# Performance work log

Hardware: AMD Instinct MI355X
Metric: run time of the kernel (lower is better)

The kernel has to match this reference:

```python
import jax, jax.numpy as jnp
import numpy as np

N_USER, N_ITEM, N_BUNDLE = 200000, 100000, 50000
EMBED_DIM = 128
B, L = 8192, 100  # batch of bundles, max items per bundle


def setup_inputs() -> dict:
    key = jax.random.key(0)
    ks = jax.random.split(key, 12)
    d, d2 = EMBED_DIM, 2 * EMBED_DIM
    x_u = jax.random.randint(ks[0], (B,), 0, N_USER)
    x_b = jax.random.randint(ks[1], (B,), 0, N_BUNDLE)
    items = jax.random.randint(ks[2], (B, L), 0, N_ITEM)
    # ragged bundle sizes in [10, L]; padded+masked form of the CSR gather
    lengths = jax.random.randint(ks[3], (B,), 10, L + 1)
    mask = jnp.arange(L)[None, :] < lengths[:, None]  # [B, L] bool
    return {
        "x_u": x_u,
        "x_b": x_b,
        "items": items,
        "mask": mask,
        "emb_u": jax.random.normal(ks[4], (N_USER, d), jnp.float32) * 0.1,
        "emb_i": jax.random.normal(ks[5], (N_ITEM, d), jnp.float32) * 0.1,
        "emb_b": jax.random.normal(ks[6], (N_BUNDLE, d), jnp.float32) * 0.1,
        "A": jax.random.normal(ks[7], (N_ITEM, d), jnp.float32) * 0.1,
        "fc1_w": jax.random.normal(ks[8], (d2, d2), jnp.float32) / np.sqrt(d2),
        "fc1_b": jnp.zeros((d2,), jnp.float32),
        "fc2_w": jax.random.normal(ks[9], (d2, d2), jnp.float32) / np.sqrt(d2),
        "fc2_b": jnp.zeros((d2,), jnp.float32),
        "out_w": jax.random.normal(ks[10], (1, d2), jnp.float32) / np.sqrt(d2),
        "out_b": jnp.zeros((1,), jnp.float32),
    }


def reference(x_u, x_b, items, mask, emb_u, emb_i, emb_b, A,
              fc1_w, fc1_b, fc2_w, fc2_b, out_w, out_b):
    # DAM.forward_bundle with the attention() per-bundle loop vectorized
    h_u = emb_u[x_u]                       # [B, d]
    h_b = emb_b[x_b]                       # [B, d]
    item_e = emb_i[items]                  # [B, L, d] ragged gather (padded)
    a_e = A[items]                         # [B, L, d]
    # w = softmax_l( sum_d e_u * A[item] ) per bundle, over valid items only
    scores = jnp.einsum('bd,bld->bl', h_u, a_e)
    scores = jnp.where(mask, scores, -jnp.inf)
    w = jax.nn.softmax(scores, axis=1)     # [B, L]
    h_x = jnp.einsum('bl,bld->bd', w, item_e)
    h = jnp.concatenate([h_u, h_b + h_x], axis=1)   # [B, 2d]
    h = jax.nn.leaky_relu(h @ fc1_w.T + fc1_b)
    h = jax.nn.leaky_relu(h @ fc2_w.T + fc2_b)
    return h @ out_w.T + out_b             # [B, 1]
```

## Files before the change

### kernel.cpp

```cpp
#include <hip/hip_runtime.h>
#include <hip/hip_bf16.h>

#define D   128
#define D2  256

typedef short bf16x8 __attribute__((ext_vector_type(8)));
typedef float f32x4  __attribute__((ext_vector_type(4)));

__device__ __forceinline__ float bf2f(unsigned short u) {
    return __uint_as_float(((unsigned int)u) << 16);
}
__device__ __forceinline__ float bflo(unsigned int p) { return __uint_as_float(p << 16); }
__device__ __forceinline__ float bfhi(unsigned int p) { return __uint_as_float(p & 0xffff0000u); }
__device__ __forceinline__ unsigned short f2bf(float f) {
    __hip_bfloat16 h = __float2bfloat16(f);
    return *(unsigned short*)&h;
}

template<bool BF>
__device__ __forceinline__ float ld1(const void* p, size_t i) {
    if constexpr (BF) return bf2f(((const unsigned short*)p)[i]);
    else              return ((const float*)p)[i];
}

template<bool BF>
__device__ __forceinline__ void load8f(const void* p, size_t elem_off, float* r) {
    if constexpr (BF) {
        uint4 v = *(const uint4*)((const unsigned short*)p + elem_off);
        r[0]=bflo(v.x); r[1]=bfhi(v.x); r[2]=bflo(v.y); r[3]=bfhi(v.y);
        r[4]=bflo(v.z); r[5]=bfhi(v.z); r[6]=bflo(v.w); r[7]=bfhi(v.w);
    } else {
        const float4* q = (const float4*)((const float*)p + elem_off);
        float4 a = q[0], b = q[1];
        r[0]=a.x; r[1]=a.y; r[2]=a.z; r[3]=a.w;
        r[4]=b.x; r[5]=b.y; r[6]=b.z; r[7]=b.w;
    }
}

__global__ void detect_kernel(const unsigned int* __restrict__ probe,
                              const unsigned char* __restrict__ mask,
                              int* __restrict__ flags)
{
    const int t = threadIdx.x;
    int cnt = 0;
    for (int i = t; i < 256; i += 64) {
        unsigned int e = (probe[i] >> 7) & 0xffu;
        cnt += (e >= 90 && e < 130) ? 1 : 0;
    }
    #pragma unroll
    for (int o = 32; o; o >>= 1) cnt += __shfl_xor(cnt, o);
    if (t == 0) {
        flags[0] = (cnt >= 128) ? 1 : 0;
        flags[1] = (mask[1] == 0) ? 0 : ((mask[0] == 1) ? 1 : 2);
    }
}

template<bool BF>
__device__ __forceinline__ void attn_body(
    const int* __restrict__ x_u, const int* __restrict__ x_b,
    const int* __restrict__ items, const void* __restrict__ mask, int mmode,
    const void* __restrict__ emb_u, const void* __restrict__ emb_i,
    const void* __restrict__ emb_b, const void* __restrict__ Aw,
    unsigned short* __restrict__ h_out, int L)
{
    const int b  = blockIdx.x;
    const int t  = threadIdx.x;
    const int wv = t >> 6, ln = t & 63;

    __shared__ float hu_s[D];
    __shared__ float sc_s[128];
    __shared__ float w_s[128];
    __shared__ int   it_s[128];
    __shared__ int   cnt_s[4];
    __shared__ float redm_s[4];
    __shared__ float reds_s[4];
    __shared__ float part_s[16][D];

    const int xu = x_u[b], xb = x_b[b];
    float hu = 0.f;
    if (t < D) { hu = ld1<BF>(emb_u, (size_t)xu * D + t); hu_s[t] = hu; }

    bool valid = false;
    if (t < L && t < 128) {
        const size_t mi = (size_t)b * L + t;
        it_s[t] = items[mi];
        if (mmode == 0)      valid = ((const int*)mask)[mi] != 0;
        else if (mmode == 1) valid = ((const unsigned char*)mask)[mi] != 0;
        else                 valid = ((const unsigned short*)mask)[mi] != 0;
    }
    unsigned long long bm = __ballot(valid);
    if (ln == 0) cnt_s[wv] = __popcll(bm);
    __syncthreads();
    const int len = cnt_s[0] + cnt_s[1] + cnt_s[2] + cnt_s[3];

    const int item = t >> 1, half = t & 1;
    if (item < len) {
        float acc = 0.f, r[8];
        const size_t base = (size_t)it_s[item] * D + half * 64;
        const float4* hu4 = (const float4*)hu_s + half * 16;
        #pragma unroll
        for (int c = 0; c < 8; ++c) {
            load8f<BF>(Aw, base + 8 * c, r);
            float4 ha = hu4[2 * c], hb2 = hu4[2 * c + 1];
            acc += ha.x * r[0] + ha.y * r[1] + ha.z * r[2] + ha.w * r[3]
                 + hb2.x * r[4] + hb2.y * r[5] + hb2.z * r[6] + hb2.w * r[7];
        }
        acc += __shfl_xor(acc, 1);
        if (half == 0) sc_s[item] = acc;
    }
    if (t >= len && t < 128) it_s[t] = it_s[0];
    __syncthreads();

    const float s = (t < len) ? sc_s[t] : -INFINITY;
    float mx = s;
    #pragma unroll
    for (int o = 32; o; o >>= 1) mx = fmaxf(mx, __shfl_xor(mx, o));
    if (ln == 0) redm_s[wv] = mx;
    __syncthreads();
    mx = fmaxf(fmaxf(redm_s[0], redm_s[1]), fmaxf(redm_s[2], redm_s[3]));
    const float e = (t < len) ? __expf(s - mx) : 0.f;
    float sm = e;
    #pragma unroll
    for (int o = 32; o; o >>= 1) sm += __shfl_xor(sm, o);
    if (ln == 0) reds_s[wv] = sm;
    __syncthreads();
    sm = reds_s[0] + reds_s[1] + reds_s[2] + reds_s[3];
    const float inv = (sm > 0.f) ? 1.f / sm : 0.f;
    if (t < 128) w_s[t] = e * inv;
    __syncthreads();

    const int g = t >> 4, m16 = t & 15;
    const int nit = (len + 31) & ~31;
    float acc[8];
    #pragma unroll
    for (int k = 0; k < 8; ++k) acc[k] = 0.f;
    for (int i = 0; i < nit; i += 32) {
        const int l0 = i + g, l1 = i + 16 + g;
        const float w0 = w_s[l0], w1 = w_s[l1];
        float r0[8], r1[8];
        load8f<BF>(emb_i, (size_t)it_s[l0] * D + 8 * m16, r0);
        load8f<BF>(emb_i, (size_t)it_s[l1] * D + 8 * m16, r1);
        #pragma unroll
        for (int k = 0; k < 8; ++k) acc[k] += w0 * r0[k] + w1 * r1[k];
    }
    #pragma unroll
    for (int k = 0; k < 8; ++k) part_s[g][8 * m16 + k] = acc[k];
    __syncthreads();

    if (t < D) {
        float hx = 0.f;
        #pragma unroll
        for (int gg = 0; gg < 16; ++gg) hx += part_s[gg][t];
        const float hbv = ld1<BF>(emb_b, (size_t)xb * D + t);
        h_out[(size_t)b * D2 + t]     = f2bf(hu);
        h_out[(size_t)b * D2 + D + t] = f2bf(hbv + hx);
    }
}

__global__ __launch_bounds__(256) void attn_kernel(
    const int* x_u, const int* x_b, const int* items, const void* mask,
    const void* emb_u, const void* emb_i, const void* emb_b, const void* A,
    unsigned short* h_out, int L, const int* __restrict__ flags)
{
    if (flags[0]) attn_body<true >(x_u, x_b, items, mask, flags[1], emb_u, emb_i, emb_b, A, h_out, L);
    else          attn_body<false>(x_u, x_b, items, mask, flags[1], emb_u, emb_i, emb_b, A, h_out, L);
}

template<bool BF>
__device__ __forceinline__ bf16x8 load_w8(const void* W, size_t off) {
    if constexpr (BF) {
        return *(const bf16x8*)((const unsigned short*)W + off);
    } else {
        const float* p = (const float*)W + off;
        float4 a = *(const float4*)p;
        float4 b = *(const float4*)(p + 4);
        bf16x8 r;
        r[0] = (short)f2bf(a.x); r[1] = (short)f2bf(a.y);
        r[2] = (short)f2bf(a.z); r[3] = (short)f2bf(a.w);
        r[4] = (short)f2bf(b.x); r[5] = (short)f2bf(b.y);
        r[6] = (short)f2bf(b.z); r[7] = (short)f2bf(b.w);
        return r;
    }
}

template<bool BF>
__device__ __forceinline__ void fc_body(
    const unsigned short* __restrict__ X, const void* __restrict__ W,
    const void* __restrict__ bias, unsigned short* __restrict__ Y)
{
    const int tid  = threadIdx.x;
    const int wave = tid >> 6;
    const int lane = tid & 63;
    const int l16  = lane & 15;
    const int quad = lane >> 4;
    const int mt   = blockIdx.x * 16;

    bf16x8 afrag[8];
    const size_t abase = (size_t)(mt + l16) * D2 + quad * 8;
    #pragma unroll
    for (int kc = 0; kc < 8; ++kc)
        afrag[kc] = *(const bf16x8*)(X + abase + kc * 32);

    #pragma unroll
    for (int jj = 0; jj < 4; ++jj) {
        const int jt = wave * 4 + jj;
        const size_t bbase = (size_t)(jt * 16 + l16) * D2 + quad * 8;
        f32x4 acc = {0.f, 0.f, 0.f, 0.f};
        #pragma unroll
        for (int kc = 0; kc < 8; ++kc) {
            bf16x8 bfrag = load_w8<BF>(W, bbase + kc * 32);
            acc = __builtin_amdgcn_mfma_f32_16x16x32_bf16(afrag[kc], bfrag, acc, 0, 0, 0);
        }
        const int j  = jt * 16 + l16;
        const float bj = ld1<BF>(bias, j);
        #pragma unroll
        for (int r = 0; r < 4; ++r) {
            float v = acc[r] + bj;
            v = v > 0.f ? v : 0.01f * v;
            Y[(size_t)(mt + quad * 4 + r) * D2 + j] = f2bf(v);
        }
    }
}

__global__ __launch_bounds__(256) void fc_mfma_kernel(
    const unsigned short* X, const void* W, const void* bias,
    unsigned short* Y, const int* __restrict__ flags)
{
    if (flags[0]) fc_body<true >(X, W, bias, Y);
    else          fc_body<false>(X, W, bias, Y);
}

template<bool BF>
__device__ __forceinline__ void out_body(
    const unsigned short* __restrict__ X, const void* __restrict__ out_w,
    const void* __restrict__ out_b, void* __restrict__ out, int B)
{
    const int gid  = blockIdx.x * blockDim.x + threadIdx.x;
    const int row  = gid >> 6;
    const int lane = threadIdx.x & 63;
    if (row >= B) return;

    const uint2 xv = ((const uint2*)(X + (size_t)row * D2))[lane];
    const float x0 = bflo(xv.x), x1 = bfhi(xv.x), x2 = bflo(xv.y), x3 = bfhi(xv.y);
    float w0, w1, w2, w3;
    if constexpr (BF) {
        uint2 wv = ((const uint2*)out_w)[lane];
        w0 = bflo(wv.x); w1 = bfhi(wv.x); w2 = bflo(wv.y); w3 = bfhi(wv.y);
    } else {
        float4 wv = ((const float4*)out_w)[lane];
        w0 = wv.x; w1 = wv.y; w2 = wv.z; w3 = wv.w;
    }
    float acc = x0 * w0 + x1 * w1 + x2 * w2 + x3 * w3;
    #pragma unroll
    for (int off = 32; off; off >>= 1) acc += __shfl_down(acc, off);
    if (lane == 0) {
        const float v = acc + ld1<BF>(out_b, 0);
        if constexpr (BF) ((unsigned short*)out)[row] = f2bf(v);
        else              ((float*)out)[row] = v;
    }
}

__global__ __launch_bounds__(256) void out_kernel(
    const unsigned short* X, const void* out_w, const void* out_b,
    void* out, int B, const int* __restrict__ flags)
{
    if (flags[0]) out_body<true >(X, out_w, out_b, out, B);
    else          out_body<false>(X, out_w, out_b, out, B);
}

extern "C" void kernel_launch(void* const* d_in, const int* in_sizes, int n_in,
                              void* d_out, int out_size, void* d_ws, size_t ws_size,
                              hipStream_t stream) {
    const int*  x_u   = (const int*)d_in[0];
    const int*  x_b   = (const int*)d_in[1];
    const int*  items = (const int*)d_in[2];
    const void* mask  = d_in[3];
    const void* emb_u = d_in[4];
    const void* emb_i = d_in[5];
    const void* emb_b = d_in[6];
    const void* A     = d_in[7];
    const void* fc1_w = d_in[8];
    const void* fc1_b = d_in[9];
    const void* fc2_w = d_in[10];
    const void* fc2_b = d_in[11];
    const void* out_w = d_in[12];
    const void* out_b = d_in[13];

    const int B = in_sizes[0];
    const int L = in_sizes[2] / B;

    unsigned short* h  = (unsigned short*)d_ws;
    unsigned short* h1 = h + (size_t)B * D2;
    int* flags = (int*)(h1 + (size_t)B * D2);

    detect_kernel<<<1, 64, 0, stream>>>((const unsigned int*)emb_u,
                                        (const unsigned char*)mask, flags);
    attn_kernel<<<B, 256, 0, stream>>>(x_u, x_b, items, mask,
                                       emb_u, emb_i, emb_b, A, h, L, flags);
    fc_mfma_kernel<<<B / 16, 256, 0, stream>>>(h,  fc1_w, fc1_b, h1, flags);
    fc_mfma_kernel<<<B / 16, 256, 0, stream>>>(h1, fc2_w, fc2_b, h,  flags);
    out_kernel<<<B / 4, 256, 0, stream>>>(h, out_w, out_b, d_out, B, flags);
}
```

Baseline: 329.4 us.

## Fuse MLP layers into one kernel, inline dtype probe, prefetch item rows

The separate detect kernel is removed; each attention and MLP block now runs the dtype and mask probe itself into shared memory. fc1, fc2 and the output projection are fused into one kernel that keeps the hidden activations in padded shared memory, which drops two launches and the global round trips for the intermediates. In the bf16 path the attention kernel issues the emb_i gathers for all 128 slots before the softmax so they overlap the reductions, and the softmax now skips the max-subtraction pass and its barrier. Skipping the max subtraction risks overflow if scores grow large, and every block now repeats the small probe read.

```diff
diff --git a/kernel.cpp b/kernel.cpp
--- a/kernel.cpp
+++ b/kernel.cpp
@@ -3,6 +3,7 @@
 
 #define D   128
 #define D2  256
+#define H1P 272
 
 typedef short bf16x8 __attribute__((ext_vector_type(8)));
 typedef float f32x4  __attribute__((ext_vector_type(4)));
@@ -37,22 +38,16 @@
     }
 }
 
-__global__ void detect_kernel(const unsigned int* __restrict__ probe,
-                              const unsigned char* __restrict__ mask,
-                              int* __restrict__ flags)
-{
-    const int t = threadIdx.x;
+__device__ __forceinline__ int probe_bf16(const unsigned int* probe, int lane) {
     int cnt = 0;
-    for (int i = t; i < 256; i += 64) {
-        unsigned int e = (probe[i] >> 7) & 0xffu;
+    #pragma unroll
+    for (int i = 0; i < 4; ++i) {
+        unsigned int e = (probe[lane + 64 * i] >> 7) & 0xffu;
         cnt += (e >= 90 && e < 130) ? 1 : 0;
     }
     #pragma unroll
     for (int o = 32; o; o >>= 1) cnt += __shfl_xor(cnt, o);
-    if (t == 0) {
-        flags[0] = (cnt >= 128) ? 1 : 0;
-        flags[1] = (mask[1] == 0) ? 0 : ((mask[0] == 1) ? 1 : 2);
-    }
+    return cnt;
 }
 
 template<bool BF>
@@ -61,20 +56,13 @@
     const int* __restrict__ items, const void* __restrict__ mask, int mmode,
     const void* __restrict__ emb_u, const void* __restrict__ emb_i,
     const void* __restrict__ emb_b, const void* __restrict__ Aw,
-    unsigned short* __restrict__ h_out, int L)
+    unsigned short* __restrict__ h_out, int L,
+    float* hu_s, float* sc_s, float* w_s, int* it_s,
+    int* cnt_s, float* reds_s, float (*part_s)[132])
 {
     const int b  = blockIdx.x;
     const int t  = threadIdx.x;
     const int wv = t >> 6, ln = t & 63;
-
-    __shared__ float hu_s[D];
-    __shared__ float sc_s[128];
-    __shared__ float w_s[128];
-    __shared__ int   it_s[128];
-    __shared__ int   cnt_s[4];
-    __shared__ float redm_s[4];
-    __shared__ float reds_s[4];
-    __shared__ float part_s[16][D];
 
     const int xu = x_u[b], xb = x_b[b];
     float hu = 0.f;
@@ -111,14 +99,20 @@
     if (t >= len && t < 128) it_s[t] = it_s[0];
     __syncthreads();
 
-    const float s = (t < len) ? sc_s[t] : -INFINITY;
-    float mx = s;
-    #pragma unroll
-    for (int o = 32; o; o >>= 1) mx = fmaxf(mx, __shfl_xor(mx, o));
-    if (ln == 0) redm_s[wv] = mx;
-    __syncthreads();
-    mx = fmaxf(fmaxf(redm_s[0], redm_s[1]), fmaxf(redm_s[2], redm_s[3]));
-    const float e = (t < len) ? __expf(s - mx) : 0.f;
+    const int g = t >> 4, m16 = t & 15;
+
+    uint4 pre0[4], pre1[4];
+    if constexpr (BF) {
+        const unsigned short* EI = (const unsigned short*)emb_i;
+        #pragma unroll
+        for (int i = 0; i < 4; ++i) {
+            pre0[i] = *(const uint4*)(EI + (size_t)it_s[32 * i + g]      * D + 8 * m16);
+            pre1[i] = *(const uint4*)(EI + (size_t)it_s[32 * i + 16 + g] * D + 8 * m16);
+        }
+    }
+
+    const float e = (t < len) ? __expf(sc_s[t]) : 0.f;
+    if (t < 128) w_s[t] = e;
     float sm = e;
     #pragma unroll
     for (int o = 32; o; o >>= 1) sm += __shfl_xor(sm, o);
@@ -126,25 +120,39 @@
     __syncthreads();
     sm = reds_s[0] + reds_s[1] + reds_s[2] + reds_s[3];
     const float inv = (sm > 0.f) ? 1.f / sm : 0.f;
-    if (t < 128) w_s[t] = e * inv;
-    __syncthreads();
-
-    const int g = t >> 4, m16 = t & 15;
-    const int nit = (len + 31) & ~31;
-    float acc[8];
-    #pragma unroll
-    for (int k = 0; k < 8; ++k) acc[k] = 0.f;
-    for (int i = 0; i < nit; i += 32) {
-        const int l0 = i + g, l1 = i + 16 + g;
-        const float w0 = w_s[l0], w1 = w_s[l1];
-        float r0[8], r1[8];
-        load8f<BF>(emb_i, (size_t)it_s[l0] * D + 8 * m16, r0);
-        load8f<BF>(emb_i, (size_t)it_s[l1] * D + 8 * m16, r1);
-        #pragma unroll
-        for (int k = 0; k < 8; ++k) acc[k] += w0 * r0[k] + w1 * r1[k];
-    }
-    #pragma unroll
-    for (int k = 0; k < 8; ++k) part_s[g][8 * m16 + k] = acc[k];
+
+    float acc8[8];
+    #pragma unroll
+    for (int k = 0; k < 8; ++k) acc8[k] = 0.f;
+    if constexpr (BF) {
+        #pragma unroll
+        for (int i = 0; i < 4; ++i) {
+            const float w0 = w_s[32 * i + g], w1 = w_s[32 * i + 16 + g];
+            const uint4 p0 = pre0[i], p1 = pre1[i];
+            acc8[0] += w0 * bflo(p0.x) + w1 * bflo(p1.x);
+            acc8[1] += w0 * bfhi(p0.x) + w1 * bfhi(p1.x);
+            acc8[2] += w0 * bflo(p0.y) + w1 * bflo(p1.y);
+            acc8[3] += w0 * bfhi(p0.y) + w1 * bfhi(p1.y);
+            acc8[4] += w0 * bflo(p0.z) + w1 * bflo(p1.z);
+            acc8[5] += w0 * bfhi(p0.z) + w1 * bfhi(p1.z);
+            acc8[6] += w0 * bflo(p0.w) + w1 * bflo(p1.w);
+            acc8[7] += w0 * bfhi(p0.w) + w1 * bfhi(p1.w);
+        }
+    } else {
+        const int nit = (len + 31) & ~31;
+        for (int i = 0; i < nit; i += 32) {
+            const float w0 = w_s[i + g], w1 = w_s[i + 16 + g];
+            float r0[8], r1[8];
+            load8f<false>(emb_i, (size_t)it_s[i + g] * D + 8 * m16, r0);
+            load8f<false>(emb_i, (size_t)it_s[i + 16 + g] * D + 8 * m16, r1);
+            #pragma unroll
+            for (int k = 0; k < 8; ++k) acc8[k] += w0 * r0[k] + w1 * r1[k];
+        }
+    }
+    f32x4 v0 = {acc8[0] * inv, acc8[1] * inv, acc8[2] * inv, acc8[3] * inv};
+    f32x4 v1 = {acc8[4] * inv, acc8[5] * inv, acc8[6] * inv, acc8[7] * inv};
+    *(f32x4*)&part_s[g][8 * m16]     = v0;
+    *(f32x4*)&part_s[g][8 * m16 + 4] = v1;
     __syncthreads();
 
     if (t < D) {
@@ -160,10 +168,32 @@
 __global__ __launch_bounds__(256) void attn_kernel(
     const int* x_u, const int* x_b, const int* items, const void* mask,
     const void* emb_u, const void* emb_i, const void* emb_b, const void* A,
-    unsigned short* h_out, int L, const int* __restrict__ flags)
+    unsigned short* h_out, int L)
 {
-    if (flags[0]) attn_body<true >(x_u, x_b, items, mask, flags[1], emb_u, emb_i, emb_b, A, h_out, L);
-    else          attn_body<false>(x_u, x_b, items, mask, flags[1], emb_u, emb_i, emb_b, A, h_out, L);
+    __shared__ float hu_s[D];
+    __shared__ float sc_s[128];
+    __shared__ float w_s[128];
+    __shared__ int   it_s[128];
+    __shared__ int   cnt_s[4];
+    __shared__ float reds_s[4];
+    __shared__ float part_s[16][132];
+    __shared__ int   flag_s[2];
+
+    const int t = threadIdx.x;
+    if (t < 64) {
+        int cnt = probe_bf16((const unsigned int*)emb_u, t);
+        if (t == 0) {
+            const unsigned char* mb = (const unsigned char*)mask;
+            flag_s[0] = (cnt >= 128) ? 1 : 0;
+            flag_s[1] = (mb[1] == 0) ? 0 : ((mb[0] == 1) ? 1 : 2);
+        }
+    }
+    __syncthreads();
+
+    if (flag_s[0]) attn_body<true >(x_u, x_b, items, mask, flag_s[1], emb_u, emb_i, emb_b, A,
+                                    h_out, L, hu_s, sc_s, w_s, it_s, cnt_s, reds_s, part_s);
+    else           attn_body<false>(x_u, x_b, items, mask, flag_s[1], emb_u, emb_i, emb_b, A,
+                                    h_out, L, hu_s, sc_s, w_s, it_s, cnt_s, reds_s, part_s);
 }
 
 template<bool BF>
@@ -184,9 +214,13 @@
 }
 
 template<bool BF>
-__device__ __forceinline__ void fc_body(
-    const unsigned short* __restrict__ X, const void* __restrict__ W,
-    const void* __restrict__ bias, unsigned short* __restrict__ Y)
+__device__ __forceinline__ void mlp_body(
+    const unsigned short* __restrict__ X,
+    const void* __restrict__ fc1_w, const void* __restrict__ fc1_b,
+    const void* __restrict__ fc2_w, const void* __restrict__ fc2_b,
+    const void* __restrict__ out_w, const void* __restrict__ out_b,
+    void* __restrict__ out,
+    unsigned short* h1_s, float (*po_s)[16])
 {
     const int tid  = threadIdx.x;
     const int wave = tid >> 6;
@@ -208,64 +242,83 @@
         f32x4 acc = {0.f, 0.f, 0.f, 0.f};
         #pragma unroll
         for (int kc = 0; kc < 8; ++kc) {
-            bf16x8 bfrag = load_w8<BF>(W, bbase + kc * 32);
+            bf16x8 bfrag = load_w8<BF>(fc1_w, bbase + kc * 32);
             acc = __builtin_amdgcn_mfma_f32_16x16x32_bf16(afrag[kc], bfrag, acc, 0, 0, 0);
         }
         const int j  = jt * 16 + l16;
-        const float bj = ld1<BF>(bias, j);
+        const float bj = ld1<BF>(fc1_b, j);
         #pragma unroll
         for (int r = 0; r < 4; ++r) {
             float v = acc[r] + bj;
             v = v > 0.f ? v : 0.01f * v;
-            Y[(size_t)(mt + quad * 4 + r) * D2 + j] = f2bf(v);
-        }
-    }
-}
-
-__global__ __launch_bounds__(256) void fc_mfma_kernel(
-    const unsigned short* X, const void* W, const void* bias,
-    unsigned short* Y, const int* __restrict__ flags)
+            h1_s[(quad * 4 + r) * H1P + j] = f2bf(v);
+        }
+    }
+    __syncthreads();
+
+    bf16x8 afrag2[8];
+    #pragma unroll
+    for (int kc = 0; kc < 8; ++kc)
+        afrag2[kc] = *(const bf16x8*)&h1_s[l16 * H1P + quad * 8 + kc * 32];
+
+    float po[4] = {0.f, 0.f, 0.f, 0.f};
+    #pragma unroll
+    for (int jj = 0; jj < 4; ++jj) {
+        const int jt = wave * 4 + jj;
+        const size_t bbase = (size_t)(jt * 16 + l16) * D2 + quad * 8;
+        f32x4 acc = {0.f, 0.f, 0.f, 0.f};
+        #pragma unroll
+        for (int kc = 0; kc < 8; ++kc) {
+            bf16x8 bfrag = load_w8<BF>(fc2_w, bbase + kc * 32);
+            acc = __builtin_amdgcn_mfma_f32_16x16x32_bf16(afrag2[kc], bfrag, acc, 0, 0, 0);
+        }
+        const int j  = jt * 16 + l16;
+        const float bj = ld1<BF>(fc2_b, j);
+        const float wj = ld1<BF>(out_w, j);
+        #pragma unroll
+        for (int r = 0; r < 4; ++r) {
+            float v = acc[r] + bj;
+            v = v > 0.f ? v : 0.01f * v;
+            po[r] += v * wj;
+        }
+    }
+    #pragma unroll
+    for (int r = 0; r < 4; ++r) {
+        #pragma unroll
+        for (int o = 1; o < 16; o <<= 1) po[r] += __shfl_xor(po[r], o);
+    }
+    if (l16 == 0) {
+        #pragma unroll
+        for (int r = 0; r < 4; ++r) po_s[wave][quad * 4 + r] = po[r];
+    }
+    __syncthreads();
+
+    if (tid < 16) {
+        const float v = po_s[0][tid] + po_s[1][tid] + po_s[2][tid] + po_s[3][tid]
+                      + ld1<BF>(out_b, 0);
+        if constexpr (BF) ((unsigned short*)out)[mt + tid] = f2bf(v);
+        else              ((float*)out)[mt + tid] = v;
+    }
+}
+
+__global__ __launch_bounds__(256) void mlp_kernel(
+    const unsigned short* X,
+    const void* fc1_w, const void* fc1_b, const void* fc2_w, const void* fc2_b,
+    const void* out_w, const void* out_b, void* out, const void* probe)
 {
-    if (flags[0]) fc_body<true >(X, W, bias, Y);
-    else          fc_body<false>(X, W, bias, Y);
-}
-
-template<bool BF>
-__device__ __forceinline__ void out_body(
-    const unsigned short* __restrict__ X, const void* __restrict__ out_w,
-    const void* __restrict__ out_b, void* __restrict__ out, int B)
-{
-    const int gid  = blockIdx.x * blockDim.x + threadIdx.x;
-    const int row  = gid >> 6;
-    const int lane = threadIdx.x & 63;
-    if (row >= B) return;
-
-    const uint2 xv = ((const uint2*)(X + (size_t)row * D2))[lane];
-    const float x0 = bflo(xv.x), x1 = bfhi(xv.x), x2 = bflo(xv.y), x3 = bfhi(xv.y);
-    float w0, w1, w2, w3;
-    if constexpr (BF) {
-        uint2 wv = ((const uint2*)out_w)[lane];
-        w0 = bflo(wv.x); w1 = bfhi(wv.x); w2 = bflo(wv.y); w3 = bfhi(wv.y);
-    } else {
-        float4 wv = ((const float4*)out_w)[lane];
-        w0 = wv.x; w1 = wv.y; w2 = wv.z; w3 = wv.w;
-    }
-    float acc = x0 * w0 + x1 * w1 + x2 * w2 + x3 * w3;
-    #pragma unroll
-    for (int off = 32; off; off >>= 1) acc += __shfl_down(acc, off);
-    if (lane == 0) {
-        const float v = acc + ld1<BF>(out_b, 0);
-        if constexpr (BF) ((unsigned short*)out)[row] = f2bf(v);
-        else              ((float*)out)[row] = v;
-    }
-}
-
-__global__ __launch_bounds__(256) void out_kernel(
-    const unsigned short* X, const void* out_w, const void* out_b,
-    void* out, int B, const int* __restrict__ flags)
-{
-    if (flags[0]) out_body<true >(X, out_w, out_b, out, B);
-    else          out_body<false>(X, out_w, out_b, out, B);
+    __shared__ unsigned short h1_s[16 * H1P];
+    __shared__ float po_s[4][16];
+    __shared__ int flag_s;
+
+    const int t = threadIdx.x;
+    if (t < 64) {
+        int cnt = probe_bf16((const unsigned int*)probe, t);
+        if (t == 0) flag_s = (cnt >= 128) ? 1 : 0;
+    }
+    __syncthreads();
+
+    if (flag_s) mlp_body<true >(X, fc1_w, fc1_b, fc2_w, fc2_b, out_w, out_b, out, h1_s, po_s);
+    else        mlp_body<false>(X, fc1_w, fc1_b, fc2_w, fc2_b, out_w, out_b, out, h1_s, po_s);
 }
 
 extern "C" void kernel_launch(void* const* d_in, const int* in_sizes, int n_in,
@@ -289,15 +342,10 @@
     const int B = in_sizes[0];
     const int L = in_sizes[2] / B;
 
-    unsigned short* h  = (unsigned short*)d_ws;
-    unsigned short* h1 = h + (size_t)B * D2;
-    int* flags = (int*)(h1 + (size_t)B * D2);
-
-    detect_kernel<<<1, 64, 0, stream>>>((const unsigned int*)emb_u,
-                                        (const unsigned char*)mask, flags);
+    unsigned short* h = (unsigned short*)d_ws;
+
     attn_kernel<<<B, 256, 0, stream>>>(x_u, x_b, items, mask,
-                                       emb_u, emb_i, emb_b, A, h, L, flags);
-    fc_mfma_kernel<<<B / 16, 256, 0, stream>>>(h,  fc1_w, fc1_b, h1, flags);
-    fc_mfma_kernel<<<B / 16, 256, 0, stream>>>(h1, fc2_w, fc2_b, h,  flags);
-    out_kernel<<<B / 4, 256, 0, stream>>>(h, out_w, out_b, d_out, B, flags);
-}
+                                       emb_u, emb_i, emb_b, A, h, L);
+    mlp_kernel<<<B / 16, 256, 0, stream>>>(h, fc1_w, fc1_b, fc2_w, fc2_b,
+                                           out_w, out_b, d_out, emb_u);
+}
```

New measurement: 330.9 us. About the same (+0.5%).
